# Kernel optimization log

Measured on AMD Instinct MI355X. Metric: run time of the kernel, lower is better.

Reference implementation:

```python
import jax, jax.numpy as jnp
import numpy as np

NUM_STATES = 64
HIDDEN = 32
NUM_ACTIONS = 3
SEQ_LEN = 512
BATCH = 2048


def setup_inputs() -> dict:
    key = jax.random.key(0)
    ks = jax.random.split(key, 7)
    s_ih = 1.0 / np.sqrt(HIDDEN)
    x = jax.random.normal(ks[0], (SEQ_LEN, BATCH, NUM_STATES), dtype=jnp.float32)
    # PyTorch LSTM params: gate order [i, f, g, o], each block of size HIDDEN
    W_ih = jax.random.uniform(ks[1], (4 * HIDDEN, NUM_STATES), minval=-s_ih, maxval=s_ih, dtype=jnp.float32)
    W_hh = jax.random.uniform(ks[2], (4 * HIDDEN, HIDDEN), minval=-s_ih, maxval=s_ih, dtype=jnp.float32)
    b_ih = jax.random.uniform(ks[3], (4 * HIDDEN,), minval=-s_ih, maxval=s_ih, dtype=jnp.float32)
    b_hh = jax.random.uniform(ks[4], (4 * HIDDEN,), minval=-s_ih, maxval=s_ih, dtype=jnp.float32)
    s_d = 1.0 / np.sqrt(HIDDEN)
    W_d = jax.random.uniform(ks[5], (NUM_ACTIONS, HIDDEN), minval=-s_d, maxval=s_d, dtype=jnp.float32)
    b_d = jax.random.uniform(ks[6], (NUM_ACTIONS,), minval=-s_d, maxval=s_d, dtype=jnp.float32)
    return {"x": x, "W_ih": W_ih, "W_hh": W_hh, "b_ih": b_ih, "b_hh": b_hh, "W_d": W_d, "b_d": b_d}


def _lstm_last_hidden(x, W_ih, W_hh, b_ih, b_hh):
    # x: [T, B, F] time-major, as in nn.LSTM(batch_first=False)
    B = x.shape[1]
    H = W_hh.shape[1]
    # Precompute input projections for all timesteps in one GEMM: [T, B, 4H]
    x_proj = jnp.einsum('tbf,gf->tbg', x, W_ih) + (b_ih + b_hh)

    def step(carry, xp_t):
        h, c = carry
        gates = xp_t + h @ W_hh.T  # [B, 4H]
        i, f, g, o = jnp.split(gates, 4, axis=-1)
        i = jax.nn.sigmoid(i)
        f = jax.nn.sigmoid(f)
        g = jnp.tanh(g)
        o = jax.nn.sigmoid(o)
        c = f * c + i * g
        h = o * jnp.tanh(c)
        return (h, c), None

    h0 = jnp.zeros((B, H), dtype=x.dtype)
    c0 = jnp.zeros((B, H), dtype=x.dtype)
    (h_T, _), _ = jax.lax.scan(step, (h0, c0), x_proj)
    return h_T  # [B, H] == lstm output at last timestep (x[-1,:,:])


def reference(x, W_ih, W_hh, b_ih, b_hh, W_d, b_d):
    h_T = _lstm_last_hidden(x, W_ih, W_hh, b_ih, b_hh)
    h = jax.nn.relu(h_T)
    return h @ W_d.T + b_d  # [B, num_actions]
```

## Files before the change

kernel.cpp:

```cpp
#include <hip/hip_runtime.h>

typedef __bf16 bf16_t;
typedef __bf16 bf16x8 __attribute__((ext_vector_type(8)));
typedef __bf16 bf16x4 __attribute__((ext_vector_type(4)));
typedef float  f32x4  __attribute__((ext_vector_type(4)));

#define T_STEPS 512
#define BATCH   2048
#define NS      64
#define HID     32
#define HSTR    40
#define FSTR    36
#define PFD     4

__device__ __forceinline__ float fast_sigmoid(float x) {
  return __builtin_amdgcn_rcpf(1.0f + __builtin_amdgcn_exp2f(-1.4426950408889634f * x));
}
__device__ __forceinline__ float fast_tanh(float x) {
  return 1.0f - 2.0f * __builtin_amdgcn_rcpf(1.0f + __builtin_amdgcn_exp2f(2.8853900817779268f * x));
}

__device__ __forceinline__ void barrier_lgkm() {
  asm volatile("s_waitcnt lgkmcnt(0)\n\ts_barrier" ::: "memory");
}

__global__ __launch_bounds__(128, 1)
void lstm_policy_kernel(const float* __restrict__ x,
                        const float* __restrict__ W_ih,
                        const float* __restrict__ W_hh,
                        const float* __restrict__ b_ih,
                        const float* __restrict__ b_hh,
                        const float* __restrict__ W_d,
                        const float* __restrict__ b_d,
                        float* __restrict__ out)
{
  __shared__ bf16_t hbuf[2][16 * HSTR];
  __shared__ float  hf[16 * FSTR];

  const int tid  = threadIdx.x;
  const int wave = tid >> 6;
  const int lane = tid & 63;
  const int m    = lane & 15;
  const int q    = lane >> 4;
  const int u0   = wave << 4;
  const int row0 = blockIdx.x << 4;

  for (int i = tid; i < 16 * HSTR; i += 128) hbuf[0][i] = (bf16_t)0.0f;

  bf16x8 a_ih[4][2], a_hh[4];
  f32x4  bias[4];
  #pragma unroll
  for (int G = 0; G < 4; ++G) {
    const int wrow = (G << 5) + u0 + m;
    const float* pih = W_ih + wrow * 64;
    const float* phh = W_hh + (wrow << 5);
    #pragma unroll
    for (int j = 0; j < 8; ++j) {
      a_ih[G][0][j] = (bf16_t)pih[(q << 3) + j];
      a_ih[G][1][j] = (bf16_t)pih[32 + (q << 3) + j];
      a_hh[G][j]    = (bf16_t)phh[(q << 3) + j];
    }
    #pragma unroll
    for (int r = 0; r < 4; ++r) {
      const int u = (G << 5) + u0 + (q << 2) + r;
      bias[G][r] = b_ih[u] + b_hh[u];
    }
  }

  const size_t xstep = (size_t)BATCH * NS;
  const float* xr = x + (size_t)(row0 + m) * NS + (q << 3);
  f32x4 xf[PFD][4];
  #pragma unroll
  for (int d = 0; d < PFD; ++d) {
    const float* p = xr + (size_t)d * xstep;
    xf[d][0] = *(const f32x4*)(p);
    xf[d][1] = *(const f32x4*)(p + 4);
    xf[d][2] = *(const f32x4*)(p + 32);
    xf[d][3] = *(const f32x4*)(p + 36);
  }

  float cst[4] = {0.0f, 0.0f, 0.0f, 0.0f};

  __syncthreads();

  #pragma unroll PFD
  for (int t = 0; t < T_STEPS; ++t) {
    const int pb = t & 1;
    const int sl = t & (PFD - 1);
    bf16x8 xA, xB;
    #pragma unroll
    for (int j = 0; j < 4; ++j) {
      xA[j]     = (bf16_t)xf[sl][0][j];
      xA[4 + j] = (bf16_t)xf[sl][1][j];
      xB[j]     = (bf16_t)xf[sl][2][j];
      xB[4 + j] = (bf16_t)xf[sl][3][j];
    }
    {
      const int tp = (t + PFD < T_STEPS) ? (t + PFD) : t;
      const float* pf = xr + (size_t)tp * xstep;
      xf[sl][0] = *(const f32x4*)(pf);
      xf[sl][1] = *(const f32x4*)(pf + 4);
      xf[sl][2] = *(const f32x4*)(pf + 32);
      xf[sl][3] = *(const f32x4*)(pf + 36);
    }
    f32x4 ai = __builtin_amdgcn_mfma_f32_16x16x32_bf16(a_ih[0][0], xA, bias[0], 0, 0, 0);
    f32x4 af = __builtin_amdgcn_mfma_f32_16x16x32_bf16(a_ih[1][0], xA, bias[1], 0, 0, 0);
    f32x4 ag = __builtin_amdgcn_mfma_f32_16x16x32_bf16(a_ih[2][0], xA, bias[2], 0, 0, 0);
    f32x4 ao = __builtin_amdgcn_mfma_f32_16x16x32_bf16(a_ih[3][0], xA, bias[3], 0, 0, 0);
    ai = __builtin_amdgcn_mfma_f32_16x16x32_bf16(a_ih[0][1], xB, ai, 0, 0, 0);
    af = __builtin_amdgcn_mfma_f32_16x16x32_bf16(a_ih[1][1], xB, af, 0, 0, 0);
    ag = __builtin_amdgcn_mfma_f32_16x16x32_bf16(a_ih[2][1], xB, ag, 0, 0, 0);
    ao = __builtin_amdgcn_mfma_f32_16x16x32_bf16(a_ih[3][1], xB, ao, 0, 0, 0);
    const bf16x8 hfr = *(const bf16x8*)(&hbuf[pb][m * HSTR + (q << 3)]);
    ai = __builtin_amdgcn_mfma_f32_16x16x32_bf16(a_hh[0], hfr, ai, 0, 0, 0);
    af = __builtin_amdgcn_mfma_f32_16x16x32_bf16(a_hh[1], hfr, af, 0, 0, 0);
    ag = __builtin_amdgcn_mfma_f32_16x16x32_bf16(a_hh[2], hfr, ag, 0, 0, 0);
    ao = __builtin_amdgcn_mfma_f32_16x16x32_bf16(a_hh[3], hfr, ao, 0, 0, 0);
    bf16x4 hv;
    #pragma unroll
    for (int r = 0; r < 4; ++r) {
      const float ig = fast_sigmoid(ai[r]);
      const float fg = fast_sigmoid(af[r]);
      const float gg = fast_tanh(ag[r]);
      const float og = fast_sigmoid(ao[r]);
      const float cn = fg * cst[r] + ig * gg;
      cst[r] = cn;
      const float h = og * fast_tanh(cn);
      hv[r] = (bf16_t)h;
      if (t == T_STEPS - 1) hf[m * FSTR + u0 + (q << 2) + r] = fmaxf(h, 0.0f);
    }
    *(bf16x4*)(&hbuf[pb ^ 1][m * HSTR + u0 + (q << 2)]) = hv;
    barrier_lgkm();
  }

  __syncthreads();

  if (tid < 48) {
    const int r = tid / 3;
    const int a = tid - r * 3;
    float s = b_d[a];
    #pragma unroll
    for (int u = 0; u < HID; ++u)
      s += hf[r * FSTR + u] * W_d[a * HID + u];
    out[(size_t)(row0 + r) * 3 + a] = s;
  }
}

extern "C" void kernel_launch(void* const* d_in, const int* in_sizes, int n_in,
                              void* d_out, int out_size, void* d_ws, size_t ws_size,
                              hipStream_t stream) {
  const float* x    = (const float*)d_in[0];
  const float* W_ih = (const float*)d_in[1];
  const float* W_hh = (const float*)d_in[2];
  const float* b_ih = (const float*)d_in[3];
  const float* b_hh = (const float*)d_in[4];
  const float* W_d  = (const float*)d_in[5];
  const float* b_d  = (const float*)d_in[6];
  float* out = (float*)d_out;

  dim3 grid(BATCH / 16);
  dim3 block(128);
  hipLaunchKernelGGL(lstm_policy_kernel, grid, block, 0, stream,
                     x, W_ih, W_hh, b_ih, b_hh, W_d, b_d, out);
}
```

Measured before the change: 540.2 us.

## Software-pipeline input projection one step ahead of recurrent MFMAs

Computes the input-projection MFMAs for step t+1 during step t, keeping double-buffered accumulators, so only the four W_hh MFMAs and gate math sit on the serial recurrence path. The loop is manually unrolled by four with compile-time buffer indices, and the prefetch ring is shifted to load five steps ahead. This shortens the per-step dependency chain but increases register pressure; the last iteration computes an unused projection from a clamped address.

```diff
diff --git a/kernel.cpp b/kernel.cpp
--- a/kernel.cpp
+++ b/kernel.cpp
@@ -11,7 +11,6 @@
 #define HID     32
 #define HSTR    40
 #define FSTR    36
-#define PFD     4
 
 __device__ __forceinline__ float fast_sigmoid(float x) {
   return __builtin_amdgcn_rcpf(1.0f + __builtin_amdgcn_exp2f(-1.4426950408889634f * x));
@@ -23,6 +22,8 @@
 __device__ __forceinline__ void barrier_lgkm() {
   asm volatile("s_waitcnt lgkmcnt(0)\n\ts_barrier" ::: "memory");
 }
+
+#define MFMA(A, B, C) __builtin_amdgcn_mfma_f32_16x16x32_bf16((A), (B), (C), 0, 0, 0)
 
 __global__ __launch_bounds__(128, 1)
 void lstm_policy_kernel(const float* __restrict__ x,
@@ -69,69 +70,95 @@
 
   const size_t xstep = (size_t)BATCH * NS;
   const float* xr = x + (size_t)(row0 + m) * NS + (q << 3);
-  f32x4 xf[PFD][4];
-  #pragma unroll
-  for (int d = 0; d < PFD; ++d) {
-    const float* p = xr + (size_t)d * xstep;
-    xf[d][0] = *(const f32x4*)(p);
-    xf[d][1] = *(const f32x4*)(p + 4);
-    xf[d][2] = *(const f32x4*)(p + 32);
-    xf[d][3] = *(const f32x4*)(p + 36);
+
+  f32x4 xf[4][4];
+  {
+    const float* p1 = xr + xstep;
+    const float* p2 = xr + 2 * xstep;
+    const float* p3 = xr + 3 * xstep;
+    const float* p4 = xr + 4 * xstep;
+    xf[1][0]=*(const f32x4*)(p1); xf[1][1]=*(const f32x4*)(p1+4); xf[1][2]=*(const f32x4*)(p1+32); xf[1][3]=*(const f32x4*)(p1+36);
+    xf[2][0]=*(const f32x4*)(p2); xf[2][1]=*(const f32x4*)(p2+4); xf[2][2]=*(const f32x4*)(p2+32); xf[2][3]=*(const f32x4*)(p2+36);
+    xf[3][0]=*(const f32x4*)(p3); xf[3][1]=*(const f32x4*)(p3+4); xf[3][2]=*(const f32x4*)(p3+32); xf[3][3]=*(const f32x4*)(p3+36);
+    xf[0][0]=*(const f32x4*)(p4); xf[0][1]=*(const f32x4*)(p4+4); xf[0][2]=*(const f32x4*)(p4+32); xf[0][3]=*(const f32x4*)(p4+36);
+  }
+
+  f32x4 acc[2][4];
+  {
+    f32x4 x0a = *(const f32x4*)(xr), x0b = *(const f32x4*)(xr + 4);
+    f32x4 x0c = *(const f32x4*)(xr + 32), x0d = *(const f32x4*)(xr + 36);
+    bf16x8 xA, xB;
+    #pragma unroll
+    for (int j = 0; j < 4; ++j) {
+      xA[j] = (bf16_t)x0a[j]; xA[4+j] = (bf16_t)x0b[j];
+      xB[j] = (bf16_t)x0c[j]; xB[4+j] = (bf16_t)x0d[j];
+    }
+    #pragma unroll
+    for (int G = 0; G < 4; ++G) {
+      acc[0][G] = MFMA(a_ih[G][0], xA, bias[G]);
+      acc[0][G] = MFMA(a_ih[G][1], xB, acc[0][G]);
+    }
   }
 
   float cst[4] = {0.0f, 0.0f, 0.0f, 0.0f};
 
   __syncthreads();
 
-  #pragma unroll PFD
-  for (int t = 0; t < T_STEPS; ++t) {
-    const int pb = t & 1;
-    const int sl = t & (PFD - 1);
-    bf16x8 xA, xB;
-    #pragma unroll
-    for (int j = 0; j < 4; ++j) {
-      xA[j]     = (bf16_t)xf[sl][0][j];
-      xA[4 + j] = (bf16_t)xf[sl][1][j];
-      xB[j]     = (bf16_t)xf[sl][2][j];
-      xB[4 + j] = (bf16_t)xf[sl][3][j];
-    }
-    {
-      const int tp = (t + PFD < T_STEPS) ? (t + PFD) : t;
-      const float* pf = xr + (size_t)tp * xstep;
-      xf[sl][0] = *(const f32x4*)(pf);
-      xf[sl][1] = *(const f32x4*)(pf + 4);
-      xf[sl][2] = *(const f32x4*)(pf + 32);
-      xf[sl][3] = *(const f32x4*)(pf + 36);
-    }
-    f32x4 ai = __builtin_amdgcn_mfma_f32_16x16x32_bf16(a_ih[0][0], xA, bias[0], 0, 0, 0);
-    f32x4 af = __builtin_amdgcn_mfma_f32_16x16x32_bf16(a_ih[1][0], xA, bias[1], 0, 0, 0);
-    f32x4 ag = __builtin_amdgcn_mfma_f32_16x16x32_bf16(a_ih[2][0], xA, bias[2], 0, 0, 0);
-    f32x4 ao = __builtin_amdgcn_mfma_f32_16x16x32_bf16(a_ih[3][0], xA, bias[3], 0, 0, 0);
-    ai = __builtin_amdgcn_mfma_f32_16x16x32_bf16(a_ih[0][1], xB, ai, 0, 0, 0);
-    af = __builtin_amdgcn_mfma_f32_16x16x32_bf16(a_ih[1][1], xB, af, 0, 0, 0);
-    ag = __builtin_amdgcn_mfma_f32_16x16x32_bf16(a_ih[2][1], xB, ag, 0, 0, 0);
-    ao = __builtin_amdgcn_mfma_f32_16x16x32_bf16(a_ih[3][1], xB, ao, 0, 0, 0);
-    const bf16x8 hfr = *(const bf16x8*)(&hbuf[pb][m * HSTR + (q << 3)]);
-    ai = __builtin_amdgcn_mfma_f32_16x16x32_bf16(a_hh[0], hfr, ai, 0, 0, 0);
-    af = __builtin_amdgcn_mfma_f32_16x16x32_bf16(a_hh[1], hfr, af, 0, 0, 0);
-    ag = __builtin_amdgcn_mfma_f32_16x16x32_bf16(a_hh[2], hfr, ag, 0, 0, 0);
-    ao = __builtin_amdgcn_mfma_f32_16x16x32_bf16(a_hh[3], hfr, ao, 0, 0, 0);
-    bf16x4 hv;
-    #pragma unroll
-    for (int r = 0; r < 4; ++r) {
-      const float ig = fast_sigmoid(ai[r]);
-      const float fg = fast_sigmoid(af[r]);
-      const float gg = fast_tanh(ag[r]);
-      const float og = fast_sigmoid(ao[r]);
-      const float cn = fg * cst[r] + ig * gg;
-      cst[r] = cn;
-      const float h = og * fast_tanh(cn);
-      hv[r] = (bf16_t)h;
-      if (t == T_STEPS - 1) hf[m * FSTR + u0 + (q << 2) + r] = fmaxf(h, 0.0f);
-    }
-    *(bf16x4*)(&hbuf[pb ^ 1][m * HSTR + u0 + (q << 2)]) = hv;
-    barrier_lgkm();
+  #define STEP(P)                                                                     \
+  do {                                                                                \
+    const int tt = t + (P);                                                           \
+                                 \
+    const bf16x8 hfr = *(const bf16x8*)(&hbuf[(P) & 1][m * HSTR + (q << 3)]);         \
+            \
+    {                                                                                 \
+      bf16x8 xA, xB;                                                                  \
+      _Pragma("unroll")                                                               \
+      for (int j = 0; j < 4; ++j) {                                                   \
+        xA[j]   = (bf16_t)xf[((P)+1)&3][0][j]; xA[4+j] = (bf16_t)xf[((P)+1)&3][1][j]; \
+        xB[j]   = (bf16_t)xf[((P)+1)&3][2][j]; xB[4+j] = (bf16_t)xf[((P)+1)&3][3][j]; \
+      }                                                                               \
+      _Pragma("unroll")                                                               \
+      for (int G = 0; G < 4; ++G) {                                                   \
+        acc[((P)+1)&1][G] = MFMA(a_ih[G][0], xA, bias[G]);                            \
+        acc[((P)+1)&1][G] = MFMA(a_ih[G][1], xB, acc[((P)+1)&1][G]);                  \
+      }                                                                               \
+      int tp = tt + 5; if (tp > T_STEPS - 1) tp = T_STEPS - 1;                        \
+      const float* pf = xr + (size_t)tp * xstep;                                      \
+      xf[((P)+1)&3][0] = *(const f32x4*)(pf);                                         \
+      xf[((P)+1)&3][1] = *(const f32x4*)(pf + 4);                                     \
+      xf[((P)+1)&3][2] = *(const f32x4*)(pf + 32);                                    \
+      xf[((P)+1)&3][3] = *(const f32x4*)(pf + 36);                                    \
+    }                                                                                 \
+                               \
+    f32x4 gi = MFMA(a_hh[0], hfr, acc[(P)&1][0]);                                     \
+    f32x4 gf = MFMA(a_hh[1], hfr, acc[(P)&1][1]);                                     \
+    f32x4 gg = MFMA(a_hh[2], hfr, acc[(P)&1][2]);                                     \
+    f32x4 go = MFMA(a_hh[3], hfr, acc[(P)&1][3]);                                     \
+    bf16x4 hv;                                                                        \
+    _Pragma("unroll")                                                                 \
+    for (int r = 0; r < 4; ++r) {                                                     \
+      const float ig = fast_sigmoid(gi[r]);                                           \
+      const float fg = fast_sigmoid(gf[r]);                                           \
+      const float gv = fast_tanh(gg[r]);                                              \
+      const float og = fast_sigmoid(go[r]);                                           \
+      const float cn = fg * cst[r] + ig * gv;                                         \
+      cst[r] = cn;                                                                    \
+      const float h = og * fast_tanh(cn);                                             \
+      hv[r] = (bf16_t)h;                                                              \
+      if (tt == T_STEPS - 1) hf[m * FSTR + u0 + (q << 2) + r] = fmaxf(h, 0.0f);       \
+    }                                                                                 \
+    *(bf16x4*)(&hbuf[((P)&1)^1][m * HSTR + u0 + (q << 2)]) = hv;                      \
+    barrier_lgkm();                                                                   \
+  } while (0)
+
+  #pragma unroll 1
+  for (int t = 0; t < T_STEPS; t += 4) {
+    STEP(0);
+    STEP(1);
+    STEP(2);
+    STEP(3);
   }
+  #undef STEP
 
   __syncthreads();
 
```

Result: faster. 504.6 us (-6.6%).
